# Kernel optimization log

Measured on AMD Instinct MI355X. Metric: run time of the kernel, lower is better.

The kernel has to match this reference:

```python
import jax, jax.numpy as jnp
import numpy as np

N_HEAD = 16

def _rope_cache(dim, T):
    # matches precompute_rope_cache: angles = outer(pos, 1/theta^(2i/dim))
    pos = jnp.arange(T, dtype=jnp.float32)
    freq = 1.0 / (10000.0 ** (jnp.arange(0, dim, 2, dtype=jnp.float32) / dim))
    ang = pos[:, None] * freq[None, :]  # (T, dim//2)
    return jnp.cos(ang), jnp.sin(ang)

def _apply_rope(x, cos, sin):
    # x: (B, H, T, hs). Faithful to the (nonstandard, roll-based) torch apply_rope,
    # including the reassignment of x_rot before it is used for x_pass.
    x_rot, x_pass = x[..., ::2], x[..., 1::2]
    c = cos[None, None]  # (1,1,T,hs//2)
    s = sin[None, None]
    new_rot = x_rot * c - jnp.roll(x_pass, 1, axis=-1) * s
    new_pass = x_pass * c + jnp.roll(new_rot, -1, axis=-1) * s
    return jnp.stack([new_rot, new_pass], axis=-1).reshape(x.shape)

def setup_inputs() -> dict:
    key = jax.random.key(0)
    k1, k2, k3 = jax.random.split(key, 3)
    B, T, C = 2, 2048, 1024
    x = jax.random.normal(k1, (B, T, C), dtype=jnp.float32)
    w_attn = jax.random.normal(k2, (3 * C, C), dtype=jnp.float32) * 0.02
    w_proj = jax.random.normal(k3, (C, C), dtype=jnp.float32) * 0.02
    return {"x": x, "w_attn": w_attn, "w_proj": w_proj}

def reference(x, w_attn, w_proj):
    B, T, C = x.shape
    H = N_HEAD
    hs = C // H
    qkv = jnp.einsum('btc,dc->btd', x, w_attn)  # fused QKV projection (no bias)
    q, k, v = jnp.split(qkv, 3, axis=-1)
    def heads(t):
        return t.reshape(B, T, H, hs).transpose(0, 2, 1, 3)  # (B,H,T,hs)
    q, k, v = heads(q), heads(k), heads(v)
    cos, sin = _rope_cache(hs, T)
    q = _apply_rope(q, cos, sin)
    k = _apply_rope(k, cos, sin)
    scores = jnp.einsum('bhqd,bhkd->bhqk', q, k) / jnp.sqrt(jnp.float32(hs))
    causal = jnp.tril(jnp.ones((T, T), dtype=bool))
    scores = jnp.where(causal[None, None], scores, -jnp.inf)
    att = jax.nn.softmax(scores, axis=-1)
    y = jnp.einsum('bhqk,bhkd->bhqd', att, v)
    y = y.transpose(0, 2, 1, 3).reshape(B, T, C)
    return jnp.einsum('btc,dc->btd', y, w_proj)
```

## Files before the change

### kernel.cpp

```cpp
#include <hip/hip_runtime.h>

#define T_SEQ 2048
#define NHEAD 16
#define HS 64

typedef __bf16 bf16x8 __attribute__((ext_vector_type(8)));
typedef float f32x4 __attribute__((ext_vector_type(4)));

__device__ __forceinline__ unsigned short f2bf(float f) {
  union { float f; unsigned int u; } v; v.f = f;
  return (unsigned short)((v.u + 0x7fffu + ((v.u >> 16) & 1u)) >> 16);
}
__device__ __forceinline__ float bf2f(unsigned short h) {
  union { unsigned int u; float f; } v; v.u = ((unsigned int)h) << 16;
  return v.f;
}
__device__ __forceinline__ bf16x8 ld_bf8(const unsigned short* p) {
  return *(const bf16x8*)p;
}
__device__ __forceinline__ void st_bf8(unsigned short* p, bf16x8 v) {
  *(bf16x8*)p = v;
}
__device__ __forceinline__ bf16x8 cvt8(float4 a, float4 b) {
  bf16x8 r;
  r[0] = (__bf16)a.x; r[1] = (__bf16)a.y; r[2] = (__bf16)a.z; r[3] = (__bf16)a.w;
  r[4] = (__bf16)b.x; r[5] = (__bf16)b.y; r[6] = (__bf16)b.z; r[7] = (__bf16)b.w;
  return r;
}

__global__ __launch_bounds__(256, 2) void gemm_bt(
    const void* __restrict__ Av, const void* __restrict__ Bv,
    float* __restrict__ Cout,
    unsigned short* __restrict__ qb, unsigned short* __restrict__ kb,
    unsigned short* __restrict__ vtb,
    int M, int N, int K, int af32, int bf32, int mode) {
  __shared__ unsigned short As[128 * 64];
  __shared__ unsigned short Bs[128 * 64];
  const int tid = threadIdx.x;
  const int wid = tid >> 6, lane = tid & 63;
  const int quad = lane >> 4, l16 = lane & 15;
  const int m0 = blockIdx.y * 128, n0 = blockIdx.x * 128;
  const int wm = (wid >> 1) * 64, wn = (wid & 1) * 64;
  const int row_in = tid >> 3;
  const int col_in = (tid & 7) * 8;
  const float* Agf = (const float*)Av + (size_t)(m0 + row_in) * K + col_in;
  const float* Bgf = (const float*)Bv + (size_t)(n0 + row_in) * K + col_in;
  const unsigned short* Agh = (const unsigned short*)Av + (size_t)(m0 + row_in) * K + col_in;
  const unsigned short* Bgh = (const unsigned short*)Bv + (size_t)(n0 + row_in) * K + col_in;
  f32x4 acc[4][4] = {};
  const int nkt = K >> 6;
  for (int kt = 0; kt < nkt; ++kt) {
    bf16x8 as8[4], bs8[4];
    if (af32) {
      #pragma unroll
      for (int j = 0; j < 4; ++j) {
        const float* p = Agf + (size_t)j * 32 * K + kt * 64;
        as8[j] = cvt8(*(const float4*)p, *(const float4*)(p + 4));
      }
    } else {
      #pragma unroll
      for (int j = 0; j < 4; ++j)
        as8[j] = ld_bf8(Agh + (size_t)j * 32 * K + kt * 64);
    }
    if (bf32) {
      #pragma unroll
      for (int j = 0; j < 4; ++j) {
        const float* p = Bgf + (size_t)j * 32 * K + kt * 64;
        bs8[j] = cvt8(*(const float4*)p, *(const float4*)(p + 4));
      }
    } else {
      #pragma unroll
      for (int j = 0; j < 4; ++j)
        bs8[j] = ld_bf8(Bgh + (size_t)j * 32 * K + kt * 64);
    }
    __syncthreads();
    #pragma unroll
    for (int j = 0; j < 4; ++j) {
      st_bf8(&As[(j * 32 + row_in) * 64 + col_in], as8[j]);
      st_bf8(&Bs[(j * 32 + row_in) * 64 + col_in], bs8[j]);
    }
    __syncthreads();
    #pragma unroll
    for (int ks = 0; ks < 2; ++ks) {
      bf16x8 af[4], bfr[4];
      #pragma unroll
      for (int mt = 0; mt < 4; ++mt)
        af[mt] = ld_bf8(&As[(wm + mt * 16 + l16) * 64 + ks * 32 + quad * 8]);
      #pragma unroll
      for (int nt = 0; nt < 4; ++nt)
        bfr[nt] = ld_bf8(&Bs[(wn + nt * 16 + l16) * 64 + ks * 32 + quad * 8]);
      #pragma unroll
      for (int mt = 0; mt < 4; ++mt)
        #pragma unroll
        for (int nt = 0; nt < 4; ++nt)
          acc[mt][nt] = __builtin_amdgcn_mfma_f32_16x16x32_bf16(af[mt], bfr[nt], acc[mt][nt], 0, 0, 0);
    }
  }
  #pragma unroll
  for (int mt = 0; mt < 4; ++mt) {
    #pragma unroll
    for (int nt = 0; nt < 4; ++nt) {
      const int n = n0 + wn + nt * 16 + l16;
      #pragma unroll
      for (int r = 0; r < 4; ++r) {
        const int m = m0 + wm + mt * 16 + quad * 4 + r;
        if (mode == 0) {
          Cout[(size_t)m * N + n] = acc[mt][nt][r];
        } else {
          const unsigned short val = f2bf(acc[mt][nt][r]);
          const int b = m >> 11, t = m & (T_SEQ - 1);
          const int which = n >> 10, c = n & 1023;
          const int h = c >> 6, d = c & 63;
          const int bh = b * NHEAD + h;
          if (which == 0)      qb[((size_t)bh * T_SEQ + t) * HS + d] = val;
          else if (which == 1) kb[((size_t)bh * T_SEQ + t) * HS + d] = val;
          else                 vtb[((size_t)bh * HS + d) * T_SEQ + t] = val;
        }
      }
    }
  }
}

__global__ __launch_bounds__(256, 1) void rope(unsigned short* __restrict__ qb,
                                               unsigned short* __restrict__ kb) {
  const int idx = blockIdx.x * 256 + threadIdx.x;
  unsigned short* buf = (idx < 65536 ? qb : kb) + (size_t)(idx & 65535) * HS;
  const int t = idx & (T_SEQ - 1);
  float x[64];
  #pragma unroll
  for (int j = 0; j < 64; ++j) x[j] = bf2f(buf[j]);
  __asm__ volatile("" ::: "memory");
  float c[32], s[32], er[32];
  #pragma unroll
  for (int i = 0; i < 32; ++i) {
    const float ang = (float)t * exp2f(-0.41524101186092029f * (float)i);
    c[i] = cosf(ang); s[i] = sinf(ang);
  }
  #pragma unroll
  for (int i = 0; i < 32; ++i)
    er[i] = x[2 * i] * c[i] - x[(2 * i + 63) & 63] * s[i];
  #pragma unroll
  for (int i = 0; i < 32; ++i) {
    const float ep = x[2 * i + 1] * c[i] + er[(i + 1) & 31] * s[i];
    buf[2 * i]     = f2bf(er[i]);
    buf[2 * i + 1] = f2bf(ep);
  }
}

__global__ __launch_bounds__(256, 2) void attn(
    const unsigned short* __restrict__ qb, const unsigned short* __restrict__ kb,
    const unsigned short* __restrict__ vt, unsigned short* __restrict__ yb) {
  __shared__ unsigned short P[4][16 * 32];
  const int bh = blockIdx.x & 31;
  const int qt = 31 - (blockIdx.x >> 5);
  const int wid = threadIdx.x >> 6, lane = threadIdx.x & 63;
  const int quad = lane >> 4, l16 = lane & 15;
  const int qrow0 = qt * 64 + wid * 16;
  const unsigned short* qptr = qb + ((size_t)bh * T_SEQ + qrow0 + l16) * HS;
  const bf16x8 aq0 = ld_bf8(qptr + quad * 8);
  const bf16x8 aq1 = ld_bf8(qptr + 32 + quad * 8);
  f32x4 O[4] = {};
  float m_i[4], l_i[4], alpha[4];
  #pragma unroll
  for (int r = 0; r < 4; ++r) { m_i[r] = -1e30f; l_i[r] = 0.f; }
  unsigned short* Pw = P[wid];
  const int nkt = qt * 2 + 2;
  for (int kt = 0; kt < nkt; ++kt) {
    const int k0 = kt * 32;
    if (k0 > qrow0 + 15) break;
    const unsigned short* kptr = kb + ((size_t)bh * T_SEQ + k0) * HS;
    const bf16x8 bk00 = ld_bf8(kptr + l16 * HS + quad * 8);
    const bf16x8 bk01 = ld_bf8(kptr + l16 * HS + 32 + quad * 8);
    const bf16x8 bk10 = ld_bf8(kptr + (16 + l16) * HS + quad * 8);
    const bf16x8 bk11 = ld_bf8(kptr + (16 + l16) * HS + 32 + quad * 8);
    f32x4 S0 = {}, S1 = {};
    S0 = __builtin_amdgcn_mfma_f32_16x16x32_bf16(aq0, bk00, S0, 0, 0, 0);
    S0 = __builtin_amdgcn_mfma_f32_16x16x32_bf16(aq1, bk01, S0, 0, 0, 0);
    S1 = __builtin_amdgcn_mfma_f32_16x16x32_bf16(aq0, bk10, S1, 0, 0, 0);
    S1 = __builtin_amdgcn_mfma_f32_16x16x32_bf16(aq1, bk11, S1, 0, 0, 0);
    #pragma unroll
    for (int r = 0; r < 4; ++r) {
      const int row_r = qrow0 + quad * 4 + r;
      const float s0 = (k0 + l16 <= row_r) ? S0[r] * 0.125f : -1e30f;
      const float s1 = (k0 + 16 + l16 <= row_r) ? S1[r] * 0.125f : -1e30f;
      float tm = fmaxf(s0, s1);
      #pragma unroll
      for (int off = 1; off < 16; off <<= 1) tm = fmaxf(tm, __shfl_xor(tm, off, 64));
      const float mnew = fmaxf(fmaxf(m_i[r], tm), -1e30f);
      alpha[r] = __expf(m_i[r] - mnew);
      const unsigned short h0 = f2bf(__expf(s0 - mnew));
      const unsigned short h1 = f2bf(__expf(s1 - mnew));
      float rs = bf2f(h0) + bf2f(h1);
      #pragma unroll
      for (int off = 1; off < 16; off <<= 1) rs += __shfl_xor(rs, off, 64);
      l_i[r] = l_i[r] * alpha[r] + rs;
      m_i[r] = mnew;
      Pw[(quad * 4 + r) * 32 + l16] = h0;
      Pw[(quad * 4 + r) * 32 + 16 + l16] = h1;
    }
    #pragma unroll
    for (int vg = 0; vg < 4; ++vg)
      #pragma unroll
      for (int r = 0; r < 4; ++r) O[vg][r] *= alpha[r];
    __asm__ volatile("s_waitcnt lgkmcnt(0)" ::: "memory");
    const bf16x8 pa = ld_bf8(&Pw[l16 * 32 + quad * 8]);
    __asm__ volatile("" ::: "memory");
    const unsigned short* vptr = vt + (size_t)bh * HS * T_SEQ + k0;
    #pragma unroll
    for (int vg = 0; vg < 4; ++vg) {
      const bf16x8 vb = ld_bf8(vptr + (size_t)(vg * 16 + l16) * T_SEQ + quad * 8);
      O[vg] = __builtin_amdgcn_mfma_f32_16x16x32_bf16(pa, vb, O[vg], 0, 0, 0);
    }
  }
  const int b = bh >> 4, h = bh & 15;
  #pragma unroll
  for (int r = 0; r < 4; ++r) {
    const float inv = 1.0f / fmaxf(l_i[r], 1e-30f);
    const int row = qrow0 + quad * 4 + r;
    #pragma unroll
    for (int vg = 0; vg < 4; ++vg)
      yb[((size_t)b * T_SEQ + row) * 1024 + h * HS + vg * 16 + l16] = f2bf(O[vg][r] * inv);
  }
}

extern "C" void kernel_launch(void* const* d_in, const int* in_sizes, int n_in,
                              void* d_out, int out_size, void* d_ws, size_t ws_size,
                              hipStream_t stream) {
  const float* x      = (const float*)d_in[0];
  const float* w_attn = (const float*)d_in[1];
  const float* w_proj = (const float*)d_in[2];
  float* out = (float*)d_out;
  unsigned short* qb = (unsigned short*)d_ws;
  unsigned short* kb = qb + (size_t)4194304;
  unsigned short* vt = kb + (size_t)4194304;
  unsigned short* yb = vt + (size_t)4194304;

  gemm_bt<<<dim3(24, 32), 256, 0, stream>>>(x, w_attn, nullptr, qb, kb, vt,
                                            4096, 3072, 1024, 1, 1, 1);
  rope<<<dim3(512), 256, 0, stream>>>(qb, kb);
  attn<<<dim3(1024), 256, 0, stream>>>(qb, kb, vt, yb);
  gemm_bt<<<dim3(8, 32), 256, 0, stream>>>(yb, w_proj, out, nullptr, nullptr, nullptr,
                                           4096, 1024, 1024, 0, 1, 0);
}
```

Baseline: 320.6 us.

## Use one-wave attention blocks with 64-wide key tiles and early V loads

Splits the attention kernel into single-wavefront blocks, each owning a 16-row query tile, so the grid has four times as many blocks and per-row causal work is balanced more finely. Each loop iteration now handles 64 keys instead of 32, issuing four QK MFMAs per step, and the V loads are moved ahead of the softmax so their latency can overlap the exp and shuffle work. The LDS staging buffer is padded to reduce bank conflicts, and the explicit waitcnt is dropped. The costs are higher register pressure from the extra K, V and score fragments, more masked work on the diagonal tile, and no K/V sharing across waves.

```diff
diff --git a/kernel.cpp b/kernel.cpp
--- a/kernel.cpp
+++ b/kernel.cpp
@@ -147,76 +147,93 @@
   }
 }
 
-__global__ __launch_bounds__(256, 2) void attn(
+__global__ __launch_bounds__(64) void attn(
     const unsigned short* __restrict__ qb, const unsigned short* __restrict__ kb,
     const unsigned short* __restrict__ vt, unsigned short* __restrict__ yb) {
-  __shared__ unsigned short P[4][16 * 32];
-  const int bh = blockIdx.x & 31;
-  const int qt = 31 - (blockIdx.x >> 5);
-  const int wid = threadIdx.x >> 6, lane = threadIdx.x & 63;
+  __shared__ __bf16 Pl[16][72];
+  const int u = blockIdx.x;
+  const int qi = 127 - (u >> 5);
+  const int bh = u & 31;
+  const int q0 = qi * 16;
+  const int lane = threadIdx.x & 63;
   const int quad = lane >> 4, l16 = lane & 15;
-  const int qrow0 = qt * 64 + wid * 16;
-  const unsigned short* qptr = qb + ((size_t)bh * T_SEQ + qrow0 + l16) * HS;
+
+  const unsigned short* qptr = qb + ((size_t)bh * T_SEQ + q0 + l16) * HS;
   const bf16x8 aq0 = ld_bf8(qptr + quad * 8);
   const bf16x8 aq1 = ld_bf8(qptr + 32 + quad * 8);
   f32x4 O[4] = {};
   float m_i[4], l_i[4], alpha[4];
   #pragma unroll
   for (int r = 0; r < 4; ++r) { m_i[r] = -1e30f; l_i[r] = 0.f; }
-  unsigned short* Pw = P[wid];
-  const int nkt = qt * 2 + 2;
-  for (int kt = 0; kt < nkt; ++kt) {
-    const int k0 = kt * 32;
-    if (k0 > qrow0 + 15) break;
-    const unsigned short* kptr = kb + ((size_t)bh * T_SEQ + k0) * HS;
-    const bf16x8 bk00 = ld_bf8(kptr + l16 * HS + quad * 8);
-    const bf16x8 bk01 = ld_bf8(kptr + l16 * HS + 32 + quad * 8);
-    const bf16x8 bk10 = ld_bf8(kptr + (16 + l16) * HS + quad * 8);
-    const bf16x8 bk11 = ld_bf8(kptr + (16 + l16) * HS + 32 + quad * 8);
-    f32x4 S0 = {}, S1 = {};
-    S0 = __builtin_amdgcn_mfma_f32_16x16x32_bf16(aq0, bk00, S0, 0, 0, 0);
-    S0 = __builtin_amdgcn_mfma_f32_16x16x32_bf16(aq1, bk01, S0, 0, 0, 0);
-    S1 = __builtin_amdgcn_mfma_f32_16x16x32_bf16(aq0, bk10, S1, 0, 0, 0);
-    S1 = __builtin_amdgcn_mfma_f32_16x16x32_bf16(aq1, bk11, S1, 0, 0, 0);
+
+  const unsigned short* kbase = kb + (size_t)bh * T_SEQ * HS;
+  const unsigned short* vbase = vt + (size_t)bh * HS * T_SEQ;
+  const int kend = q0 + 15;
+
+  for (int k0 = 0; k0 <= kend; k0 += 64) {
+    bf16x8 bk[4][2];
+    #pragma unroll
+    for (int t = 0; t < 4; ++t) {
+      const unsigned short* kp = kbase + (size_t)(k0 + t * 16 + l16) * HS;
+      bk[t][0] = ld_bf8(kp + quad * 8);
+      bk[t][1] = ld_bf8(kp + 32 + quad * 8);
+    }
+    f32x4 S[4] = {};
+    #pragma unroll
+    for (int t = 0; t < 4; ++t) {
+      S[t] = __builtin_amdgcn_mfma_f32_16x16x32_bf16(aq0, bk[t][0], S[t], 0, 0, 0);
+      S[t] = __builtin_amdgcn_mfma_f32_16x16x32_bf16(aq1, bk[t][1], S[t], 0, 0, 0);
+    }
+    bf16x8 vb[2][4];
+    #pragma unroll
+    for (int c = 0; c < 2; ++c)
+      #pragma unroll
+      for (int vg = 0; vg < 4; ++vg)
+        vb[c][vg] = ld_bf8(vbase + (size_t)(vg * 16 + l16) * T_SEQ + k0 + c * 32 + quad * 8);
     #pragma unroll
     for (int r = 0; r < 4; ++r) {
-      const int row_r = qrow0 + quad * 4 + r;
-      const float s0 = (k0 + l16 <= row_r) ? S0[r] * 0.125f : -1e30f;
-      const float s1 = (k0 + 16 + l16 <= row_r) ? S1[r] * 0.125f : -1e30f;
-      float tm = fmaxf(s0, s1);
+      const int row = q0 + quad * 4 + r;
+      float s[4];
+      #pragma unroll
+      for (int t = 0; t < 4; ++t)
+        s[t] = (k0 + t * 16 + l16 <= row) ? S[t][r] * 0.125f : -1e30f;
+      float tm = fmaxf(fmaxf(s[0], s[1]), fmaxf(s[2], s[3]));
       #pragma unroll
       for (int off = 1; off < 16; off <<= 1) tm = fmaxf(tm, __shfl_xor(tm, off, 64));
-      const float mnew = fmaxf(fmaxf(m_i[r], tm), -1e30f);
+      const float mnew = fmaxf(m_i[r], tm);
       alpha[r] = __expf(m_i[r] - mnew);
-      const unsigned short h0 = f2bf(__expf(s0 - mnew));
-      const unsigned short h1 = f2bf(__expf(s1 - mnew));
-      float rs = bf2f(h0) + bf2f(h1);
+      unsigned short h[4];
+      float rs = 0.f;
+      #pragma unroll
+      for (int t = 0; t < 4; ++t) {
+        h[t] = f2bf(__expf(s[t] - mnew));
+        rs += bf2f(h[t]);
+      }
       #pragma unroll
       for (int off = 1; off < 16; off <<= 1) rs += __shfl_xor(rs, off, 64);
       l_i[r] = l_i[r] * alpha[r] + rs;
       m_i[r] = mnew;
-      Pw[(quad * 4 + r) * 32 + l16] = h0;
-      Pw[(quad * 4 + r) * 32 + 16 + l16] = h1;
+      #pragma unroll
+      for (int t = 0; t < 4; ++t)
+        Pl[quad * 4 + r][t * 16 + l16] = __builtin_bit_cast(__bf16, h[t]);
     }
     #pragma unroll
     for (int vg = 0; vg < 4; ++vg)
       #pragma unroll
       for (int r = 0; r < 4; ++r) O[vg][r] *= alpha[r];
-    __asm__ volatile("s_waitcnt lgkmcnt(0)" ::: "memory");
-    const bf16x8 pa = ld_bf8(&Pw[l16 * 32 + quad * 8]);
-    __asm__ volatile("" ::: "memory");
-    const unsigned short* vptr = vt + (size_t)bh * HS * T_SEQ + k0;
-    #pragma unroll
-    for (int vg = 0; vg < 4; ++vg) {
-      const bf16x8 vb = ld_bf8(vptr + (size_t)(vg * 16 + l16) * T_SEQ + quad * 8);
-      O[vg] = __builtin_amdgcn_mfma_f32_16x16x32_bf16(pa, vb, O[vg], 0, 0, 0);
+    #pragma unroll
+    for (int c = 0; c < 2; ++c) {
+      const bf16x8 pa = *(const bf16x8*)&Pl[l16][c * 32 + quad * 8];
+      #pragma unroll
+      for (int vg = 0; vg < 4; ++vg)
+        O[vg] = __builtin_amdgcn_mfma_f32_16x16x32_bf16(pa, vb[c][vg], O[vg], 0, 0, 0);
     }
   }
   const int b = bh >> 4, h = bh & 15;
   #pragma unroll
   for (int r = 0; r < 4; ++r) {
     const float inv = 1.0f / fmaxf(l_i[r], 1e-30f);
-    const int row = qrow0 + quad * 4 + r;
+    const int row = q0 + quad * 4 + r;
     #pragma unroll
     for (int vg = 0; vg < 4; ++vg)
       yb[((size_t)b * T_SEQ + row) * 1024 + h * HS + vg * 16 + l16] = f2bf(O[vg][r] * inv);
@@ -238,7 +255,7 @@
   gemm_bt<<<dim3(24, 32), 256, 0, stream>>>(x, w_attn, nullptr, qb, kb, vt,
                                             4096, 3072, 1024, 1, 1, 1);
   rope<<<dim3(512), 256, 0, stream>>>(qb, kb);
-  attn<<<dim3(1024), 256, 0, stream>>>(qb, kb, vt, yb);
+  attn<<<dim3(4096), 64, 0, stream>>>(qb, kb, vt, yb);
   gemm_bt<<<dim3(8, 32), 256, 0, stream>>>(yb, w_proj, out, nullptr, nullptr, nullptr,
                                            4096, 1024, 1024, 0, 1, 0);
 }
```

Measured after the change: 305.8 us. -4.6%, faster.
